# Performance work log

Hardware: AMD Instinct MI355X
Metric: run time of the kernel (lower is better)

Reference implementation:

```python
import jax, jax.numpy as jnp
import numpy as np

N_NODES = 80000
N_EDGES = 1280000
IN_C, HID_C, OUT_C = 3, 64, 3
BN_EPS = 1e-5
LEAKY_SLOPE = 0.01  # torch LeakyReLU default
SELF_LOOP_W = 2.0   # GCNConv(improved=True) fill value


def gcn_conv(x, src, dst, n, W, b):
    # PyG GCNConv: x = x @ W, then degree-normalized aggregation with
    # self-loops of weight 2 (improved=True), then + bias.
    h = x @ W  # [N, out]
    deg = jnp.zeros((n,), x.dtype).at[dst].add(1.0) + SELF_LOOP_W  # in-degree + self loop weight
    dinv = jax.lax.rsqrt(deg)
    norm = dinv[src] * dinv[dst]  # per-edge norm (edge_weight = 1)
    agg = jax.ops.segment_sum(h[src] * norm[:, None], dst, num_segments=n)
    self_term = (SELF_LOOP_W * dinv * dinv)[:, None] * h  # self-loop contribution
    return agg + self_term + b


def batch_norm(x, gamma, beta):
    # training-mode BN over the node dimension, biased variance, eps=1e-5
    mean = jnp.mean(x, axis=0)
    var = jnp.mean((x - mean) ** 2, axis=0)
    return (x - mean) * jax.lax.rsqrt(var + BN_EPS) * gamma + beta


def maxpool1d(x, k, p):
    # torch MaxPool1d on a 2D [N, C] tensor pools along C (same-size: stride 1)
    return jax.lax.reduce_window(x, -jnp.inf, jax.lax.max,
                                 (1, k), (1, 1), ((0, 0), (p, p)))


def leaky_relu(x):
    return jnp.where(x >= 0, x, LEAKY_SLOPE * x)


def stage(x, src, dst, n, W, b, gamma, beta, lw, lb, pool_k, pool_p):
    h = gcn_conv(x, src, dst, n, W, b)
    h = batch_norm(h, gamma, beta)
    h = leaky_relu(maxpool1d(h, pool_k, pool_p))
    h = leaky_relu(h @ lw.T + lb)
    return h  # Dropout: eval-mode identity


def setup_inputs() -> dict:
    key = jax.random.key(0)
    ks = jax.random.split(key, 24)
    x = jax.random.normal(ks[0], (N_NODES, IN_C), dtype=jnp.float32)
    edge_index = jax.random.randint(ks[1], (2, N_EDGES), 0, N_NODES, dtype=jnp.int64)

    def lin_init(k, fan_in, shape):
        bound = 1.0 / np.sqrt(fan_in)
        return jax.random.uniform(k, shape, jnp.float32, -bound, bound)

    dims = [(IN_C, HID_C), (HID_C, HID_C), (HID_C, OUT_C)]
    params = {}
    i = 2
    for s, (cin, cout) in enumerate(dims):
        params[f"w{s}"] = lin_init(ks[i], cin, (cin, cout)); i += 1
        params[f"b{s}"] = jnp.zeros((cout,), jnp.float32)
        params[f"g{s}"] = jnp.ones((cout,), jnp.float32)
        params[f"bb{s}"] = jnp.zeros((cout,), jnp.float32)
        params[f"lw{s}"] = lin_init(ks[i], cout, (cout, cout)); i += 1
        params[f"lb{s}"] = lin_init(ks[i], cout, (cout,)); i += 1
    return {"x": x, "edge_index": edge_index, **params}


def reference(x, edge_index, w0, b0, g0, bb0, lw0, lb0,
              w1, b1, g1, bb1, lw1, lb1,
              w2, b2, g2, bb2, lw2, lb2):
    src, dst = edge_index[0], edge_index[1]
    n = x.shape[0]
    h = stage(x, src, dst, n, w0, b0, g0, bb0, lw0, lb0, 3, 1)
    h = stage(h, src, dst, n, w1, b1, g1, bb1, lw1, lb1, 5, 2)
    h = stage(h, src, dst, n, w2, b2, g2, bb2, lw2, lb2, 3, 1)
    return h
```

## Files before the change

kernel.cpp:

```cpp
#include <hip/hip_runtime.h>
#include <hip/hip_bf16.h>
#include <math.h>

#define N_NODES 80000
#define N_EDGES 1280000
#define NCB 64
#define CB_DIV 1250
#define CB_CAP 21000
#define NFB 1250
#define FB_CAP 1280
#define EPB 1280
#define ATS 20

typedef __hip_bfloat16 bf16;

__device__ __forceinline__ float leaky(float x) { return x >= 0.f ? x : 0.01f * x; }

__device__ __forceinline__ float readlane_f(float v, int l) {
    return __int_as_float(__builtin_amdgcn_readlane(__float_as_int(v), l));
}

union U4 { uint4 v; bf16 h[8]; };


__global__ void k_init(float* bnsums, float* bnrep, int* ctails, int* ftails,
                       const float* __restrict__ lw0, const float* __restrict__ w1,
                       const float* __restrict__ lw1, uint4* __restrict__ pkw) {
    int i = blockIdx.x * 256 + threadIdx.x;
    if (i < 384) bnsums[i] = 0.f;
    if (i < 2048) bnrep[i] = 0.f;
    if (i < NCB) ctails[i] = 0;
    if (i < NFB) ftails[i] = 0;
    if (i >= 1536) return;
    int set = i >> 9, r = i & 511;
    int k = r >> 3, cg = r & 7;
    U4 u;
    if (set == 0) {
#pragma unroll
        for (int j = 0; j < 8; ++j) u.h[j] = __float2bfloat16(lw0[(cg * 8 + j) * 64 + k]);
    } else if (set == 1) {
#pragma unroll
        for (int j = 0; j < 8; ++j) u.h[j] = __float2bfloat16(w1[k * 64 + cg * 8 + j]);
    } else {
#pragma unroll
        for (int j = 0; j < 8; ++j) u.h[j] = __float2bfloat16(lw1[(cg * 8 + j) * 64 + k]);
    }
    pkw[i] = u.v;
}

__global__ void __launch_bounds__(256)
k_part(const int* __restrict__ ei, unsigned int* __restrict__ cpairs,
       int* __restrict__ ctails) {
    __shared__ unsigned int s_rec[EPB];
    __shared__ int cnt[NCB], lcl[NCB], lpos[NCB], off[NCB];
    int t = threadIdx.x;
    if (t < NCB) cnt[t] = 0;
    __syncthreads();
    int base = blockIdx.x * EPB;
    unsigned int loc[5];
    int blk[5];
#pragma unroll
    for (int u = 0; u < 5; ++u) {
        int e = base + u * 256 + t;
        int s = ei[e], d = ei[N_EDGES + e];
        int b = d / CB_DIV;
        blk[u] = b;
        loc[u] = (unsigned int)s | ((unsigned int)(d - b * CB_DIV) << 17);
        atomicAdd(&cnt[b], 1);
    }
    __syncthreads();
    if (t == 0) {
        int s = 0;
        for (int q = 0; q < NCB; ++q) { lcl[q] = s; s += cnt[q]; }
    }
    if (t < NCB && cnt[t] > 0) off[t] = atomicAdd(&ctails[t], cnt[t]);
    __syncthreads();
    if (t < NCB) lpos[t] = lcl[t];
    __syncthreads();
#pragma unroll
    for (int u = 0; u < 5; ++u) {
        int b = blk[u];
        int p = atomicAdd(&lpos[b], 1);
        s_rec[p] = loc[u];
    }
    __syncthreads();
    int wv = t >> 6, ln = t & 63;
    for (int q = wv; q < NCB; q += 4) {
        int c = cnt[q];
        if (c == 0) continue;
        unsigned int* dst = cpairs + (size_t)q * CB_CAP + off[q];
        const unsigned int* src = s_rec + lcl[q];
        for (int i = ln; i < c; i += 64) dst[i] = src[i];
    }
}

__global__ void __launch_bounds__(256)
k_refine(const unsigned int* __restrict__ cpairs, const int* __restrict__ ctails,
         int* __restrict__ ftails, unsigned int* __restrict__ fpairs) {
    __shared__ unsigned int s_ed[2048];
    __shared__ unsigned int s_comp[2048];
    __shared__ int cnt2[32], off2[32], lcl[32], lpos[32];
    int b = blockIdx.x & 63;
    int j = blockIdx.x >> 6;
    int t = threadIdx.x;
    int cnt = ctails[b];
    int s0 = j * 2048;
    if (s0 >= cnt) return;
    int n = min(2048, cnt - s0);
    int fb0 = (b * CB_DIV) >> 6;
    int nbins = (((b + 1) * CB_DIV - 1) >> 6) - fb0 + 1;
    int dbase = b * CB_DIV;
    const unsigned int* lst = cpairs + (size_t)b * CB_CAP + s0;
    for (int i = t; i < n; i += 256) s_ed[i] = lst[i];
    if (t < 32) cnt2[t] = 0;
    __syncthreads();
    for (int i = t; i < n; i += 256) {
        int d = dbase + (int)(s_ed[i] >> 17);
        atomicAdd(&cnt2[(d >> 6) - fb0], 1);
    }
    __syncthreads();
    if (t == 0) {
        int s = 0;
        for (int q = 0; q < nbins; ++q) { lcl[q] = s; s += cnt2[q]; }
    }
    if (t < nbins && cnt2[t] > 0) off2[t] = atomicAdd(&ftails[fb0 + t], cnt2[t]);
    __syncthreads();
    if (t < nbins) lpos[t] = lcl[t];
    __syncthreads();
    for (int i = t; i < n; i += 256) {
        unsigned int r = s_ed[i];
        int d = dbase + (int)(r >> 17);
        int fbl = (d >> 6) - fb0;
        int p = atomicAdd(&lpos[fbl], 1);
        s_comp[p] = (r & 0x1FFFFu) | ((unsigned int)(d & 63) << 20);
    }
    __syncthreads();
    int wv = t >> 6, ln = t & 63;
    for (int q = wv; q < nbins; q += 4) {
        int c = cnt2[q];
        if (c == 0) continue;
        unsigned int* dst = fpairs + (size_t)(fb0 + q) * FB_CAP + off2[q];
        const unsigned int* src = s_comp + lcl[q];
        for (int i = ln; i < c; i += 64) dst[i] = src[i];
    }
}

__global__ void __launch_bounds__(256)
k_sortfine(const unsigned int* __restrict__ fpairs, const int* __restrict__ ftails,
           int* __restrict__ src4, float* __restrict__ dinv, int* __restrict__ cursor,
           const float* __restrict__ x, const float* __restrict__ W0,
           bf16* __restrict__ hs) {
    __shared__ unsigned int stage[FB_CAP];
    __shared__ int hist[64], cur[64];
    __shared__ float sx[192], sW0[192], sdv[64];
    __shared__ int psum[4];
    int fb = blockIdx.x;
    int t = threadIdx.x;
    int lane = t & 63, wv = t >> 6;
    int cnt = ftails[fb];
    int node0 = fb * 64;
    const unsigned int* lst = fpairs + (size_t)fb * FB_CAP;
    if (t < 64) hist[t] = 0;
    if (t >= 64 && t < 256) sW0[t - 64] = W0[t - 64];
    __syncthreads();
    int part = 0;
    for (int i = t; i < fb; i += 256) part += ftails[i];
    for (int i = t; i < cnt; i += 256)
        atomicAdd(&hist[lst[i] >> 20], 1);
    for (int i = t; i < 192; i += 256) sx[i] = x[(size_t)node0 * 3 + i];
#pragma unroll
    for (int d = 32; d > 0; d >>= 1) part += __shfl_down(part, d, 64);
    if (lane == 0) psum[wv] = part;
    __syncthreads();
    if (t < 64) {
        int base = psum[0] + psum[1] + psum[2] + psum[3];
        int h = hist[t];
        int p = h;
#pragma unroll
        for (int d = 1; d < 64; d <<= 1) {
            int q = __shfl_up(p, d, 64);
            if (t >= d) p += q;
        }
        int excl = p - h;
        cur[t] = excl;
        cursor[node0 + t] = base + excl;
        float dv = rsqrtf((float)h + 2.0f);
        dinv[node0 + t] = dv;
        sdv[t] = dv;
    }
    __syncthreads();
    for (int i = t; i < cnt; i += 256) {
        unsigned int r = lst[i];
        int p = atomicAdd(&cur[r >> 20], 1);
        stage[p] = r;
    }
    __syncthreads();
    int base = psum[0] + psum[1] + psum[2] + psum[3];
    for (int i = t; i < cnt; i += 256)
        src4[base + i] = (int)(stage[i] & 0xFFFFFu);
    for (int i = t; i < 4096; i += 256) {
        int v = i >> 6, c = i & 63;
        float h = sx[v * 3] * sW0[c] + sx[v * 3 + 1] * sW0[64 + c] + sx[v * 3 + 2] * sW0[128 + c];
        hs[(size_t)(node0 + v) * 64 + c] = __float2bfloat16(sdv[v] * h);
    }
}


__global__ void __launch_bounds__(512)
k_aggc(const bf16* __restrict__ hs, const int* __restrict__ src4,
       const int* __restrict__ cursor, const float* __restrict__ dinv,
       const float* __restrict__ bias, float* __restrict__ y,
       float* __restrict__ bnrep) {
    __shared__ float selfbuf[8][8][64];
    int t = threadIdx.x, lane = t & 63, w = t >> 6;
    int v0 = (blockIdx.x * 8 + w) * 8;
    float bc = bias[lane];
    float bs = 0.f, bss = 0.f;

    int cidx = v0 + lane;
    int cval = (lane <= 8) ? ((cidx < N_NODES) ? cursor[cidx] : N_EDGES) : 0;
    float dval = (lane < 8) ? dinv[cidx] : 0.f;
#pragma unroll
    for (int i = 0; i < 8; ++i)
        selfbuf[w][i][lane] = __bfloat162float(hs[(size_t)(v0 + i) * 64 + lane]);

    int s0 = __builtin_amdgcn_readlane(cval, 0);
    int s8 = __builtin_amdgcn_readlane(cval, 8);
    int r = 0;
    int rend = __builtin_amdgcn_readlane(cval, 1);
    float acc = 0.f;
    int e = s0;
    while (e < s8) {
        int sv[32];
        float gv[32];
        if (e + 32 <= s8) {
#pragma unroll
            for (int u = 0; u < 32; ++u) sv[u] = src4[e + u];
        } else {
#pragma unroll
            for (int u = 0; u < 32; ++u) sv[u] = src4[min(e + u, N_EDGES - 1)];
        }
#pragma unroll
        for (int u = 0; u < 32; ++u)
            gv[u] = __bfloat162float(hs[(size_t)sv[u] * 64 + lane]);
#pragma unroll
        for (int u = 0; u < 32; ++u) {
            int eu = e + u;
            if (eu < s8) {
                while (eu >= rend) {
                    float selfv = selfbuf[w][r][lane];
                    float dvc = readlane_f(dval, r);
                    float yf = fmaf(dvc, acc + 2.f * selfv, bc);
                    y[(size_t)(v0 + r) * 64 + lane] = yf;
                    bs += yf; bss += yf * yf;
                    acc = 0.f;
                    ++r;
                    rend = __builtin_amdgcn_readlane(cval, r + 1);
                }
                acc += gv[u];
            }
        }
        e += 32;
    }
    while (r < 8) {
        float selfv = selfbuf[w][r][lane];
        float dvc = readlane_f(dval, r);
        float yf = fmaf(dvc, acc + 2.f * selfv, bc);
        y[(size_t)(v0 + r) * 64 + lane] = yf;
        bs += yf; bss += yf * yf;
        acc = 0.f;
        ++r;
    }

    __shared__ float s1[512], s2[512];
    s1[t] = bs;
    s2[t] = bss;
    __syncthreads();
    if (t < 64) {
        float t1 = 0.f, t2 = 0.f;
#pragma unroll
        for (int q = 0; q < 8; ++q) {
            t1 += s1[t + q * 64];
            t2 += s2[t + q * 64];
        }
        float* dst = bnrep + (blockIdx.x & 7) * 128;
        atomicAdd(&dst[t], t1);
        atomicAdd(&dst[64 + t], t2);
    }
}

template <int P, int MODE>
__global__ void __launch_bounds__(256)
k_post64(const float* __restrict__ y, const float* __restrict__ dinv,
         const float* __restrict__ bnrep,
         const float* __restrict__ g, const float* __restrict__ bb,
         const uint4* __restrict__ lwpk, const float* __restrict__ lb,
         const uint4* __restrict__ Wnpk, const float* __restrict__ Wnf,
         bf16* __restrict__ hsout, float4* __restrict__ hs3) {
    __shared__ float s_aT[4][64 * ATS];
    __shared__ uint4 s_lwT4[64 * 8];
    __shared__ uint4 s_Wn4[MODE == 0 ? 64 * 8 : 1];
    __shared__ float s_Wnf[MODE == 1 ? 64 * 3 : 1];
    int t = threadIdx.x;
    int w = t >> 6, lane = t & 63;
    for (int i = t; i < 512; i += 256) s_lwT4[i] = lwpk[i];
    if constexpr (MODE == 0) {
        for (int i = t; i < 512; i += 256) s_Wn4[i] = Wnpk[i];
    } else {
        for (int i = t; i < 64 * 3; i += 256) s_Wnf[i] = Wnf[i];
    }
    float msum = 0.f, vsum = 0.f;
#pragma unroll
    for (int r = 0; r < 8; ++r) {
        msum += bnrep[r * 128 + lane];
        vsum += bnrep[r * 128 + 64 + lane];
    }
    float inv_n = 1.0f / (float)N_NODES;
    float mean = msum * inv_n;
    float var = fmaxf(vsum * inv_n - mean * mean, 0.f);
    float sc = g[lane] * rsqrtf(var + 1e-5f);
    float sh = bb[lane] - mean * sc;
    int c0 = (lane >> 3) * 8, n0 = (lane & 7) * 2;
    int cg0 = lane >> 3;
    float lbv[8];
#pragma unroll
    for (int i = 0; i < 8; ++i) lbv[i] = lb[c0 + i];
    float* aT = s_aT[w];

    for (int tile = blockIdx.x; tile < N_NODES / 64; tile += gridDim.x) {
        int nbase = tile * 64 + w * 16;
        __syncthreads();
#pragma unroll 4
        for (int i = 0; i < 16; ++i) {
            size_t idx = (size_t)(nbase + i) * 64 + lane;
            float z = fmaf(sc, y[idx], sh);
            float m = z;
#pragma unroll
            for (int d = 1; d <= P; ++d) {
                float up = __shfl(z, lane + d);
                float dn = __shfl(z, lane - d);
                m = fmaxf(m, (lane + d < 64) ? up : -INFINITY);
                m = fmaxf(m, (lane - d >= 0) ? dn : -INFINITY);
            }
            aT[lane * ATS + i] = leaky(m);
        }
        __syncthreads();
        float acc[2][8];
#pragma unroll
        for (int nn = 0; nn < 2; ++nn)
#pragma unroll
            for (int i = 0; i < 8; ++i) acc[nn][i] = lbv[i];
#pragma unroll 8
        for (int k = 0; k < 64; ++k) {
            float2 av = *(const float2*)&aT[k * ATS + n0];
            U4 u; u.v = s_lwT4[k * 8 + cg0];
            float a2[2] = {av.x, av.y};
            float wv[8];
#pragma unroll
            for (int i = 0; i < 8; ++i) wv[i] = __bfloat162float(u.h[i]);
#pragma unroll
            for (int nn = 0; nn < 2; ++nn)
#pragma unroll
                for (int i = 0; i < 8; ++i) acc[nn][i] = fmaf(a2[nn], wv[i], acc[nn][i]);
        }
#pragma unroll
        for (int nn = 0; nn < 2; ++nn)
#pragma unroll
            for (int i = 0; i < 8; ++i) acc[nn][i] = leaky(acc[nn][i]);

#pragma unroll
        for (int i = 0; i < 8; ++i) {
            float2 ov = make_float2(acc[0][i], acc[1][i]);
            *(float2*)&aT[(c0 + i) * ATS + n0] = ov;
        }
        if constexpr (MODE == 0) {
            float acc2[2][8];
#pragma unroll
            for (int nn = 0; nn < 2; ++nn)
#pragma unroll
                for (int i = 0; i < 8; ++i) acc2[nn][i] = 0.f;
#pragma unroll 8
            for (int k = 0; k < 64; ++k) {
                float2 av = *(const float2*)&aT[k * ATS + n0];
                U4 u; u.v = s_Wn4[k * 8 + cg0];
                float a2[2] = {av.x, av.y};
                float wv[8];
#pragma unroll
                for (int i = 0; i < 8; ++i) wv[i] = __bfloat162float(u.h[i]);
#pragma unroll
                for (int nn = 0; nn < 2; ++nn)
#pragma unroll
                    for (int i = 0; i < 8; ++i) acc2[nn][i] = fmaf(a2[nn], wv[i], acc2[nn][i]);
            }
#pragma unroll
            for (int nn = 0; nn < 2; ++nn) {
                int node = nbase + n0 + nn;
                float dv = dinv[node];
                bf16 pk[8];
#pragma unroll
                for (int i = 0; i < 8; ++i) pk[i] = __float2bfloat16(dv * acc2[nn][i]);
                *(uint4*)&hsout[(size_t)node * 64 + c0] = *(uint4*)pk;
            }
        } else {
            float acc3[2][3];
#pragma unroll
            for (int nn = 0; nn < 2; ++nn)
#pragma unroll
                for (int j = 0; j < 3; ++j) acc3[nn][j] = 0.f;
#pragma unroll 8
            for (int k = 0; k < 64; ++k) {
                float2 av = *(const float2*)&aT[k * ATS + n0];
                float a2[2] = {av.x, av.y};
                float w0 = s_Wnf[k * 3 + 0], w1 = s_Wnf[k * 3 + 1], w2v = s_Wnf[k * 3 + 2];
#pragma unroll
                for (int nn = 0; nn < 2; ++nn) {
                    acc3[nn][0] = fmaf(a2[nn], w0, acc3[nn][0]);
                    acc3[nn][1] = fmaf(a2[nn], w1, acc3[nn][1]);
                    acc3[nn][2] = fmaf(a2[nn], w2v, acc3[nn][2]);
                }
            }
            if (c0 == 0) {
#pragma unroll
                for (int nn = 0; nn < 2; ++nn) {
                    int node = nbase + n0 + nn;
                    float dv = dinv[node];
                    hs3[node] = make_float4(dv * acc3[nn][0], dv * acc3[nn][1],
                                            dv * acc3[nn][2], 0.f);
                }
            }
        }
    }
}

__global__ void __launch_bounds__(256)
k_agg3(const float4* __restrict__ hs3, const int* __restrict__ cursor,
       const int* __restrict__ src4, const float* __restrict__ dinv,
       const float* __restrict__ b2, float4* __restrict__ y3,
       float* __restrict__ bnsum) {
    int v = blockIdx.x * blockDim.x + threadIdx.x;
    float y0 = 0.f, y1 = 0.f, y2 = 0.f;
    bool valid = v < N_NODES;
    if (valid) {
        int start = cursor[v];
        int end = (v + 1 < N_NODES) ? cursor[v + 1] : N_EDGES;
        float a0 = 0.f, a1 = 0.f, a2 = 0.f;
        int e = start;
        for (; e + 4 <= end; e += 4) {
            int c[4];
#pragma unroll
            for (int u = 0; u < 4; ++u) c[u] = src4[e + u];
#pragma unroll
            for (int u = 0; u < 4; ++u) {
                float4 h = hs3[c[u]];
                a0 += h.x; a1 += h.y; a2 += h.z;
            }
        }
        for (; e < end; ++e) {
            float4 h = hs3[src4[e]];
            a0 += h.x; a1 += h.y; a2 += h.z;
        }
        float dv = dinv[v];
        float4 hsv = hs3[v];
        y0 = dv * (a0 + 2.f * hsv.x) + b2[0];
        y1 = dv * (a1 + 2.f * hsv.y) + b2[1];
        y2 = dv * (a2 + 2.f * hsv.z) + b2[2];
        y3[v] = make_float4(y0, y1, y2, 0.f);
    }
    __shared__ float sm[256];
    float vals[6] = {y0, y1, y2, y0 * y0, y1 * y1, y2 * y2};
    for (int c = 0; c < 6; ++c) {
        sm[threadIdx.x] = valid ? vals[c] : 0.f;
        __syncthreads();
        for (int off = 128; off > 0; off >>= 1) {
            if (threadIdx.x < off) sm[threadIdx.x] += sm[threadIdx.x + off];
            __syncthreads();
        }
        if (threadIdx.x == 0) atomicAdd(&bnsum[c], sm[0]);
        __syncthreads();
    }
}

__global__ void k_post3(const float4* __restrict__ y3, const float* __restrict__ bnsum,
                        const float* __restrict__ g, const float* __restrict__ bb,
                        const float* __restrict__ lw, const float* __restrict__ lb,
                        float* __restrict__ out) {
    int v = blockIdx.x * blockDim.x + threadIdx.x;
    if (v >= N_NODES) return;
    float inv_n = 1.0f / (float)N_NODES;
    float sc[3], sh[3];
#pragma unroll
    for (int c = 0; c < 3; ++c) {
        float mean = bnsum[c] * inv_n;
        float var = fmaxf(bnsum[3 + c] * inv_n - mean * mean, 0.f);
        sc[c] = g[c] * rsqrtf(var + 1e-5f);
        sh[c] = bb[c] - mean * sc[c];
    }
    float4 y = y3[v];
    float z0 = fmaf(y.x, sc[0], sh[0]);
    float z1 = fmaf(y.y, sc[1], sh[1]);
    float z2 = fmaf(y.z, sc[2], sh[2]);
    float p0 = fmaxf(z0, z1);
    float p1 = fmaxf(p0, z2);
    float p2 = fmaxf(z1, z2);
    float a0 = leaky(p0), a1 = leaky(p1), a2 = leaky(p2);
    float o0 = leaky(lb[0] + a0 * lw[0] + a1 * lw[1] + a2 * lw[2]);
    float o1 = leaky(lb[1] + a0 * lw[3] + a1 * lw[4] + a2 * lw[5]);
    float o2 = leaky(lb[2] + a0 * lw[6] + a1 * lw[7] + a2 * lw[8]);
    out[v * 3 + 0] = o0;
    out[v * 3 + 1] = o1;
    out[v * 3 + 2] = o2;
}


extern "C" void kernel_launch(void* const* d_in, const int* in_sizes, int n_in,
                              void* d_out, int out_size, void* d_ws, size_t ws_size,
                              hipStream_t stream) {
    const float* x  = (const float*)d_in[0];
    const int*   ei = (const int*)d_in[1];
    const float* w0 = (const float*)d_in[2];
    const float* b0 = (const float*)d_in[3];
    const float* g0 = (const float*)d_in[4];
    const float* bb0 = (const float*)d_in[5];
    const float* lw0 = (const float*)d_in[6];
    const float* lb0 = (const float*)d_in[7];
    const float* w1 = (const float*)d_in[8];
    const float* b1 = (const float*)d_in[9];
    const float* g1 = (const float*)d_in[10];
    const float* bb1 = (const float*)d_in[11];
    const float* lw1 = (const float*)d_in[12];
    const float* lb1 = (const float*)d_in[13];
    const float* w2 = (const float*)d_in[14];
    const float* b2 = (const float*)d_in[15];
    const float* g2 = (const float*)d_in[16];
    const float* bb2 = (const float*)d_in[17];
    const float* lw2 = (const float*)d_in[18];
    const float* lb2 = (const float*)d_in[19];
    float* out = (float*)d_out;

    char* w = (char*)d_ws;
    float* yagg = (float*)w;       w += (size_t)N_NODES * 64 * 4;
    int* src4 = (int*)w;           w += (size_t)N_EDGES * 8;
    unsigned int* fpairs = (unsigned int*)w; w += (size_t)NFB * FB_CAP * 4;
    bf16* hs = (bf16*)w;           w += (size_t)N_NODES * 64 * 2;
    float4* hs3 = (float4*)w;      w += (size_t)N_NODES * 16;
    float4* y3 = (float4*)w;       w += (size_t)N_NODES * 16;
    int* fbase = (int*)w;          w += (size_t)N_NODES * 4;
    float* dinv = (float*)w;       w += (size_t)N_NODES * 4;
    int* cursor = (int*)w;         w += (size_t)N_NODES * 4;
    int* partial = (int*)w;        w += 512 * 4;
    float* bnsum = (float*)w;      w += 384 * 4;
    int* ctails = (int*)w;         w += NCB * 4;
    int* ftails = (int*)w;         w += NFB * 4;
    (void)partial;
    unsigned int* cpairs = (unsigned int*)yagg;
    uint4* pkw = (uint4*)y3;
    float* bnrep = (float*)((char*)fbase + 16384);

    const int NB = (N_NODES + 255) / 256;

    k_init<<<8, 256, 0, stream>>>(bnsum, bnrep, ctails, ftails, lw0, w1, lw1, pkw);
    k_part<<<N_EDGES / EPB, 256, 0, stream>>>(ei, cpairs, ctails);
    k_refine<<<64 * 16, 256, 0, stream>>>(cpairs, ctails, ftails, fpairs);
    k_sortfine<<<NFB, 256, 0, stream>>>(fpairs, ftails, src4, dinv, cursor,
                                        x, w0, hs);

    k_aggc<<<1250, 512, 0, stream>>>(hs, src4, cursor, dinv, b0, yagg, bnrep);
    k_post64<1, 0><<<1250, 256, 0, stream>>>(yagg, dinv, bnrep, g0, bb0,
                                             pkw, lb0, pkw + 512, nullptr,
                                             hs, nullptr);

    k_aggc<<<1250, 512, 0, stream>>>(hs, src4, cursor, dinv, b1, yagg, bnrep + 1024);
    k_post64<2, 1><<<1250, 256, 0, stream>>>(yagg, dinv, bnrep + 1024, g1, bb1,
                                             pkw + 1024, lb1, nullptr, w2,
                                             nullptr, hs3);

    k_agg3<<<NB, 256, 0, stream>>>(hs3, cursor, src4, dinv, b2, y3, bnsum + 256);
    k_post3<<<NB, 256, 0, stream>>>(y3, bnsum + 256, g2, bb2, lw2, lb2, out);
}
```

Measured before the change: 297.7 us.

## Use bf16 MFMA for per-node 64x64 linear layers in post kernel

Replaces the scalar FMA loops for the 64x64 linear and next-layer weight products with 16x16x32 bf16 MFMA instructions. Weights are repacked into MFMA B-fragment layout and held in registers, and activations are staged in shared memory as bf16 rather than transposed fp32. The final 64-to-3 projection now uses a cross-lane shuffle reduction. Activations are rounded to bf16 before the first matmul, which adds precision loss, and several extra block barriers are introduced.

```diff
diff --git a/kernel.cpp b/kernel.cpp
--- a/kernel.cpp
+++ b/kernel.cpp
@@ -10,14 +10,20 @@
 #define NFB 1250
 #define FB_CAP 1280
 #define EPB 1280
-#define ATS 20
 
 typedef __hip_bfloat16 bf16;
+typedef __attribute__((ext_vector_type(8))) short bf16x8;
+typedef __attribute__((ext_vector_type(4))) float f32x4;
 
 __device__ __forceinline__ float leaky(float x) { return x >= 0.f ? x : 0.01f * x; }
 
 __device__ __forceinline__ float readlane_f(float v, int l) {
     return __int_as_float(__builtin_amdgcn_readlane(__float_as_int(v), l));
+}
+
+__device__ __forceinline__ short bf16bits(float x) {
+    bf16 b = __float2bfloat16(x);
+    return *(short*)&b;
 }
 
 union U4 { uint4 v; bf16 h[8]; };
@@ -33,17 +39,20 @@
     if (i < NFB) ftails[i] = 0;
     if (i >= 1536) return;
     int set = i >> 9, r = i & 511;
-    int k = r >> 3, cg = r & 7;
+    int lane = r & 63;
+    int ks = (r >> 6) & 1, ct = r >> 7;
+    int kbase = ks * 32 + (lane >> 4) * 8;
+    int c = ct * 16 + (lane & 15);
     U4 u;
     if (set == 0) {
 #pragma unroll
-        for (int j = 0; j < 8; ++j) u.h[j] = __float2bfloat16(lw0[(cg * 8 + j) * 64 + k]);
+        for (int j = 0; j < 8; ++j) u.h[j] = __float2bfloat16(lw0[c * 64 + kbase + j]);
     } else if (set == 1) {
 #pragma unroll
-        for (int j = 0; j < 8; ++j) u.h[j] = __float2bfloat16(w1[k * 64 + cg * 8 + j]);
+        for (int j = 0; j < 8; ++j) u.h[j] = __float2bfloat16(w1[(kbase + j) * 64 + c]);
     } else {
 #pragma unroll
-        for (int j = 0; j < 8; ++j) u.h[j] = __float2bfloat16(lw1[(cg * 8 + j) * 64 + k]);
+        for (int j = 0; j < 8; ++j) u.h[j] = __float2bfloat16(lw1[c * 64 + kbase + j]);
     }
     pkw[i] = u.v;
 }
@@ -297,17 +306,24 @@
          const uint4* __restrict__ lwpk, const float* __restrict__ lb,
          const uint4* __restrict__ Wnpk, const float* __restrict__ Wnf,
          bf16* __restrict__ hsout, float4* __restrict__ hs3) {
-    __shared__ float s_aT[4][64 * ATS];
-    __shared__ uint4 s_lwT4[64 * 8];
-    __shared__ uint4 s_Wn4[MODE == 0 ? 64 * 8 : 1];
-    __shared__ float s_Wnf[MODE == 1 ? 64 * 3 : 1];
-    int t = threadIdx.x;
-    int w = t >> 6, lane = t & 63;
-    for (int i = t; i < 512; i += 256) s_lwT4[i] = lwpk[i];
+    __shared__ short s_a[4][16][72];
+    __shared__ float s_Wnf[MODE == 1 ? 192 : 1];
+    int t = threadIdx.x, w = t >> 6, lane = t & 63;
+    bf16x8 bw[4][2];
+#pragma unroll
+    for (int ct = 0; ct < 4; ++ct)
+#pragma unroll
+        for (int ks = 0; ks < 2; ++ks)
+            bw[ct][ks] = *(const bf16x8*)&lwpk[(ct * 2 + ks) * 64 + lane];
+    bf16x8 wn[4][2];
     if constexpr (MODE == 0) {
-        for (int i = t; i < 512; i += 256) s_Wn4[i] = Wnpk[i];
+#pragma unroll
+        for (int ct = 0; ct < 4; ++ct)
+#pragma unroll
+            for (int ks = 0; ks < 2; ++ks)
+                wn[ct][ks] = *(const bf16x8*)&Wnpk[(ct * 2 + ks) * 64 + lane];
     } else {
-        for (int i = t; i < 64 * 3; i += 256) s_Wnf[i] = Wnf[i];
+        for (int i = t; i < 192; i += 256) s_Wnf[i] = Wnf[i];
     }
     float msum = 0.f, vsum = 0.f;
 #pragma unroll
@@ -320,20 +336,17 @@
     float var = fmaxf(vsum * inv_n - mean * mean, 0.f);
     float sc = g[lane] * rsqrtf(var + 1e-5f);
     float sh = bb[lane] - mean * sc;
-    int c0 = (lane >> 3) * 8, n0 = (lane & 7) * 2;
-    int cg0 = lane >> 3;
-    float lbv[8];
-#pragma unroll
-    for (int i = 0; i < 8; ++i) lbv[i] = lb[c0 + i];
-    float* aT = s_aT[w];
+    float lbv[4];
+#pragma unroll
+    for (int ct = 0; ct < 4; ++ct) lbv[ct] = lb[ct * 16 + (lane & 15)];
+    int row = lane & 15, kg = lane >> 4;
+    __syncthreads();
 
     for (int tile = blockIdx.x; tile < N_NODES / 64; tile += gridDim.x) {
         int nbase = tile * 64 + w * 16;
-        __syncthreads();
 #pragma unroll 4
         for (int i = 0; i < 16; ++i) {
-            size_t idx = (size_t)(nbase + i) * 64 + lane;
-            float z = fmaf(sc, y[idx], sh);
+            float z = fmaf(sc, y[(size_t)(nbase + i) * 64 + lane], sh);
             float m = z;
 #pragma unroll
             for (int d = 1; d <= P; ++d) {
@@ -342,92 +355,93 @@
                 m = fmaxf(m, (lane + d < 64) ? up : -INFINITY);
                 m = fmaxf(m, (lane - d >= 0) ? dn : -INFINITY);
             }
-            aT[lane * ATS + i] = leaky(m);
+            s_a[w][i][lane] = bf16bits(leaky(m));
         }
         __syncthreads();
-        float acc[2][8];
-#pragma unroll
-        for (int nn = 0; nn < 2; ++nn)
-#pragma unroll
-            for (int i = 0; i < 8; ++i) acc[nn][i] = lbv[i];
-#pragma unroll 8
-        for (int k = 0; k < 64; ++k) {
-            float2 av = *(const float2*)&aT[k * ATS + n0];
-            U4 u; u.v = s_lwT4[k * 8 + cg0];
-            float a2[2] = {av.x, av.y};
-            float wv[8];
-#pragma unroll
-            for (int i = 0; i < 8; ++i) wv[i] = __bfloat162float(u.h[i]);
-#pragma unroll
-            for (int nn = 0; nn < 2; ++nn)
-#pragma unroll
-                for (int i = 0; i < 8; ++i) acc[nn][i] = fmaf(a2[nn], wv[i], acc[nn][i]);
-        }
-#pragma unroll
-        for (int nn = 0; nn < 2; ++nn)
-#pragma unroll
-            for (int i = 0; i < 8; ++i) acc[nn][i] = leaky(acc[nn][i]);
-
-#pragma unroll
-        for (int i = 0; i < 8; ++i) {
-            float2 ov = make_float2(acc[0][i], acc[1][i]);
-            *(float2*)&aT[(c0 + i) * ATS + n0] = ov;
-        }
+        f32x4 acc[4];
+#pragma unroll
+        for (int ct = 0; ct < 4; ++ct) acc[ct] = (f32x4){0.f, 0.f, 0.f, 0.f};
+#pragma unroll
+        for (int ks = 0; ks < 2; ++ks) {
+            bf16x8 af = *(bf16x8*)&s_a[w][row][ks * 32 + kg * 8];
+#pragma unroll
+            for (int ct = 0; ct < 4; ++ct)
+                acc[ct] = __builtin_amdgcn_mfma_f32_16x16x32_bf16(af, bw[ct][ks], acc[ct], 0, 0, 0);
+        }
+        float o[4][4];
+#pragma unroll
+        for (int ct = 0; ct < 4; ++ct)
+#pragma unroll
+            for (int j = 0; j < 4; ++j)
+                o[ct][j] = leaky(acc[ct][j] + lbv[ct]);
+
         if constexpr (MODE == 0) {
-            float acc2[2][8];
-#pragma unroll
-            for (int nn = 0; nn < 2; ++nn)
-#pragma unroll
-                for (int i = 0; i < 8; ++i) acc2[nn][i] = 0.f;
-#pragma unroll 8
-            for (int k = 0; k < 64; ++k) {
-                float2 av = *(const float2*)&aT[k * ATS + n0];
-                U4 u; u.v = s_Wn4[k * 8 + cg0];
-                float a2[2] = {av.x, av.y};
-                float wv[8];
-#pragma unroll
-                for (int i = 0; i < 8; ++i) wv[i] = __bfloat162float(u.h[i]);
-#pragma unroll
-                for (int nn = 0; nn < 2; ++nn)
-#pragma unroll
-                    for (int i = 0; i < 8; ++i) acc2[nn][i] = fmaf(a2[nn], wv[i], acc2[nn][i]);
+            __syncthreads();
+#pragma unroll
+            for (int ct = 0; ct < 4; ++ct)
+#pragma unroll
+                for (int j = 0; j < 4; ++j)
+                    s_a[w][kg * 4 + j][ct * 16 + (lane & 15)] = bf16bits(o[ct][j]);
+            __syncthreads();
+            f32x4 acc2[4];
+#pragma unroll
+            for (int ct = 0; ct < 4; ++ct) acc2[ct] = (f32x4){0.f, 0.f, 0.f, 0.f};
+#pragma unroll
+            for (int ks = 0; ks < 2; ++ks) {
+                bf16x8 af = *(bf16x8*)&s_a[w][row][ks * 32 + kg * 8];
+#pragma unroll
+                for (int ct = 0; ct < 4; ++ct)
+                    acc2[ct] = __builtin_amdgcn_mfma_f32_16x16x32_bf16(af, wn[ct][ks], acc2[ct], 0, 0, 0);
             }
-#pragma unroll
-            for (int nn = 0; nn < 2; ++nn) {
-                int node = nbase + n0 + nn;
-                float dv = dinv[node];
-                bf16 pk[8];
-#pragma unroll
-                for (int i = 0; i < 8; ++i) pk[i] = __float2bfloat16(dv * acc2[nn][i]);
-                *(uint4*)&hsout[(size_t)node * 64 + c0] = *(uint4*)pk;
-            }
+            float dvj[4];
+#pragma unroll
+            for (int j = 0; j < 4; ++j) dvj[j] = dinv[nbase + kg * 4 + j];
+            __syncthreads();
+#pragma unroll
+            for (int ct = 0; ct < 4; ++ct)
+#pragma unroll
+                for (int j = 0; j < 4; ++j)
+                    s_a[w][kg * 4 + j][ct * 16 + (lane & 15)] = bf16bits(dvj[j] * acc2[ct][j]);
+            __syncthreads();
+            int nd = lane >> 2, c0 = (lane & 3) * 8;
+#pragma unroll
+            for (int pass = 0; pass < 2; ++pass)
+                *(uint4*)&hsout[(size_t)(nbase + nd) * 64 + c0 + pass * 32] =
+                    *(uint4*)&s_a[w][nd][c0 + pass * 32];
         } else {
-            float acc3[2][3];
-#pragma unroll
-            for (int nn = 0; nn < 2; ++nn)
-#pragma unroll
-                for (int j = 0; j < 3; ++j) acc3[nn][j] = 0.f;
-#pragma unroll 8
-            for (int k = 0; k < 64; ++k) {
-                float2 av = *(const float2*)&aT[k * ATS + n0];
-                float a2[2] = {av.x, av.y};
-                float w0 = s_Wnf[k * 3 + 0], w1 = s_Wnf[k * 3 + 1], w2v = s_Wnf[k * 3 + 2];
-#pragma unroll
-                for (int nn = 0; nn < 2; ++nn) {
-                    acc3[nn][0] = fmaf(a2[nn], w0, acc3[nn][0]);
-                    acc3[nn][1] = fmaf(a2[nn], w1, acc3[nn][1]);
-                    acc3[nn][2] = fmaf(a2[nn], w2v, acc3[nn][2]);
+            float p[4][3];
+#pragma unroll
+            for (int j = 0; j < 4; ++j)
+#pragma unroll
+                for (int m = 0; m < 3; ++m) p[j][m] = 0.f;
+            int myc = lane & 15;
+#pragma unroll
+            for (int ct = 0; ct < 4; ++ct) {
+                int ch = ct * 16 + myc;
+                float w0 = s_Wnf[ch * 3 + 0], w1 = s_Wnf[ch * 3 + 1], w2v = s_Wnf[ch * 3 + 2];
+#pragma unroll
+                for (int j = 0; j < 4; ++j) {
+                    p[j][0] = fmaf(o[ct][j], w0, p[j][0]);
+                    p[j][1] = fmaf(o[ct][j], w1, p[j][1]);
+                    p[j][2] = fmaf(o[ct][j], w2v, p[j][2]);
                 }
             }
-            if (c0 == 0) {
-#pragma unroll
-                for (int nn = 0; nn < 2; ++nn) {
-                    int node = nbase + n0 + nn;
+#pragma unroll
+            for (int mask = 1; mask <= 8; mask <<= 1)
+#pragma unroll
+                for (int j = 0; j < 4; ++j)
+#pragma unroll
+                    for (int m = 0; m < 3; ++m)
+                        p[j][m] += __shfl_xor(p[j][m], mask, 64);
+            if (myc == 0) {
+#pragma unroll
+                for (int j = 0; j < 4; ++j) {
+                    int node = nbase + kg * 4 + j;
                     float dv = dinv[node];
-                    hs3[node] = make_float4(dv * acc3[nn][0], dv * acc3[nn][1],
-                                            dv * acc3[nn][2], 0.f);
+                    hs3[node] = make_float4(dv * p[j][0], dv * p[j][1], dv * p[j][2], 0.f);
                 }
             }
+            __syncthreads();
         }
     }
 }
```

Result: faster. 267.8 us, median of 2 (-10.0%).
